# Kernel tuning notes

Hardware: AMD Instinct MI355X
Metric: run time of the kernel (lower is better)

The kernel has to match this reference:

```python
import jax, jax.numpy as jnp
import numpy as np

B, N, F, C = 8, 256, 59, 128
BOX = 20.0
EPS = 1e-5


def _bn(y, g, b, m, v):
    # eval-mode BatchNorm1d over the channel (last) axis
    return (y - m) * jax.lax.rsqrt(v + EPS) * g + b


def setup_inputs() -> dict:
    key = jax.random.key(0)
    ks = jax.random.split(key, 12)
    x = jax.random.normal(ks[0], (B, N, F), jnp.float32)
    pos = jax.random.uniform(ks[1], (B, N, 3), jnp.float32) * BOX
    nrm = jax.random.normal(ks[2], (B, N, 3), jnp.float32)
    normal = nrm / jnp.linalg.norm(nrm, axis=-1, keepdims=True)
    s_in = 1.0 / np.sqrt(F)
    W_lin = jax.random.normal(ks[3], (C, F), jnp.float32) * s_in
    W_src = jax.random.normal(ks[4], (C, F), jnp.float32) * s_in
    W_dst = jax.random.normal(ks[5], (C, F), jnp.float32) * s_in
    pos_w = jax.random.normal(ks[6], (C, 6), jnp.float32) * (1.0 / np.sqrt(6.0))
    pos_b = jax.random.normal(ks[7], (C,), jnp.float32) * 0.02
    attn_w = jax.random.normal(ks[8], (C, C), jnp.float32) * (1.0 / np.sqrt(C))
    attn_b = jax.random.normal(ks[9], (C,), jnp.float32) * 0.02
    pos_bn_g = 1.0 + 0.1 * jax.random.normal(ks[10], (C,), jnp.float32)
    attn_bn_g = 1.0 + 0.1 * jax.random.normal(ks[11], (C,), jnp.float32)
    zeros = jnp.zeros((C,), jnp.float32)
    ones = jnp.ones((C,), jnp.float32)
    return {
        'x': x, 'pos': pos, 'normal': normal,
        'W_lin': W_lin, 'W_src': W_src, 'W_dst': W_dst,
        'pos_w': pos_w, 'pos_b': pos_b,
        'pos_bn_g': pos_bn_g, 'pos_bn_b': zeros, 'pos_bn_m': zeros, 'pos_bn_v': ones,
        'attn_w': attn_w, 'attn_b': attn_b,
        'attn_bn_g': attn_bn_g, 'attn_bn_b': zeros, 'attn_bn_m': zeros, 'attn_bn_v': ones,
        'r': 5,
    }


def reference(x, pos, normal, W_lin, W_src, W_dst, pos_w, pos_b,
              pos_bn_g, pos_bn_b, pos_bn_m, pos_bn_v,
              attn_w, attn_b, attn_bn_g, attn_bn_b, attn_bn_m, attn_bn_v, r):
    r = jnp.float32(r)
    # linear projections (bias-free, as in PyG PointTransformerConv)
    v = jnp.einsum('bnf,cf->bnc', x, W_lin)      # values
    a_src = jnp.einsum('bnf,cf->bnc', x, W_src)  # alpha for source j
    a_dst = jnp.einsum('bnf,cf->bnc', x, W_dst)  # alpha for dest   i
    # relative geometry, axis 1 = receiver i, axis 2 = sender j
    rel_pos = pos[:, :, None, :] - pos[:, None, :, :]          # [B,i,j,3]
    rel_nrm = normal[:, :, None, :] - normal[:, None, :, :]    # [B,i,j,3]
    relf = jnp.concatenate([rel_pos, rel_nrm], axis=-1)        # [B,i,j,6]
    # pos_nn = Linear(6,C) + BN + ReLU (eval)
    delta = jax.nn.relu(_bn(jnp.einsum('bijk,ck->bijc', relf, pos_w) + pos_b,
                            pos_bn_g, pos_bn_b, pos_bn_m, pos_bn_v))
    # attn_nn(alpha_i - alpha_j + delta)
    alpha_arg = a_dst[:, :, None, :] - a_src[:, None, :, :] + delta
    scores = jax.nn.relu(_bn(jnp.einsum('bijc,dc->bijd', alpha_arg, attn_w) + attn_b,
                             attn_bn_g, attn_bn_b, attn_bn_m, attn_bn_v))
    # radius mask within each graph (self-loops included, dist 0 <= r)
    dist2 = jnp.sum(rel_pos * rel_pos, axis=-1)                # [B,i,j]
    mask = (dist2 <= r * r)[..., None]                         # [B,i,j,1]
    attn = jax.nn.softmax(jnp.where(mask, scores, -jnp.inf), axis=2)
    # per-channel vector attention over neighbors j: sum_j attn * (v_j + delta)
    out = jnp.sum(attn * (v[:, None, :, :] + delta), axis=2)   # [B,i,C]
    return out
```

## Files before the change

kernel.cpp:

```cpp
#include <hip/hip_runtime.h>

#define BB 8
#define NN 256
#define FF 59
#define CC 128
#define EPSV 1e-5f

#define WS_V     0
#define WS_ASRC  (WS_V + BB*NN*CC)
#define WS_ADST  (WS_ASRC + BB*NN*CC)
#define WS_PWT   (WS_ADST + BB*NN*CC)
#define WS_T1    (WS_PWT + 6*CC)
#define WS_T2    (WS_T1 + CC)
#define WS_WT    (WS_T2 + CC)

__global__ __launch_bounds__(256) void prep_kernel(
    const float* __restrict__ x, const float* __restrict__ W_lin,
    const float* __restrict__ W_src, const float* __restrict__ W_dst,
    const float* __restrict__ pos_w, const float* __restrict__ pos_b,
    const float* __restrict__ pos_g, const float* __restrict__ pos_bb,
    const float* __restrict__ pos_m, const float* __restrict__ pos_v,
    const float* __restrict__ attn_w, const float* __restrict__ attn_b,
    const float* __restrict__ attn_g, const float* __restrict__ attn_bb,
    const float* __restrict__ attn_m, const float* __restrict__ attn_v,
    float* __restrict__ ws)
{
    int blk = blockIdx.x;
    int tid = threadIdx.x;
    if (blk < 384) {
        int type = blk >> 7;
        int g    = blk & 127;
        int b    = g >> 4;
        int n0   = (g & 15) * 16;
        const float* W = (type == 0) ? W_lin : (type == 1) ? W_src : W_dst;
        float* outp = ws + ((type == 0) ? WS_V : (type == 1) ? WS_ASRC : WS_ADST);
        __shared__ float Wl[CC * FF];
        __shared__ float xs[16 * FF];
        for (int idx = tid; idx < CC * FF; idx += 256) Wl[idx] = W[idx];
        const float* xrow = x + (size_t)(b * NN + n0) * FF;
        for (int idx = tid; idx < 16 * FF; idx += 256) xs[idx] = xrow[idx];
        __syncthreads();
        int c = tid & 127, h = tid >> 7;
        float acc[8];
#pragma unroll
        for (int q = 0; q < 8; ++q) acc[q] = 0.f;
        for (int f = 0; f < FF; ++f) {
            float w = Wl[c * FF + f];
#pragma unroll
            for (int q = 0; q < 8; ++q) acc[q] += w * xs[(h * 8 + q) * FF + f];
        }
#pragma unroll
        for (int q = 0; q < 8; ++q) {
            int n = n0 + h * 8 + q;
            outp[(b * NN + n) * CC + c] = acc[q];
        }
    } else {
        __shared__ float S2s[CC];
        if (tid < CC) {
            int c = tid;
            float S1 = rsqrtf(pos_v[c] + EPSV) * pos_g[c];
            ws[WS_T1 + c] = (pos_b[c] - pos_m[c]) * S1 + pos_bb[c];
#pragma unroll
            for (int k = 0; k < 6; ++k) ws[WS_PWT + k * CC + c] = pos_w[c * 6 + k] * S1;
            float S2 = rsqrtf(attn_v[c] + EPSV) * attn_g[c];
            S2s[c] = S2;
            ws[WS_T2 + c] = (attn_b[c] - attn_m[c]) * S2 + attn_bb[c];
        }
        __syncthreads();
        for (int idx = tid; idx < CC * CC; idx += 256) {
            int d = idx & 127, cc2 = idx >> 7;
            ws[WS_WT + cc2 * CC + d] = attn_w[d * CC + cc2] * S2s[d];
        }
    }
}

__global__ __launch_bounds__(256) void main_kernel(
    const float* __restrict__ pos, const float* __restrict__ nrm,
    const int* __restrict__ rptr, const float* __restrict__ ws,
    float* __restrict__ out)
{
    const float* v    = ws + WS_V;
    const float* asrc = ws + WS_ASRC;
    const float* adst = ws + WS_ADST;
    const float* pwt  = ws + WS_PWT;
    const float* T1   = ws + WS_T1;
    const float* T2   = ws + WS_T2;
    const float* wt   = ws + WS_WT;

    int blk = blockIdx.x;
    int b = blk >> 8, i = blk & 255;
    int tid = threadIdx.x;

    __shared__ float relf[NN * 6];
    __shared__ int   jlist[NN];
    __shared__ int   wcnt[4];
    __shared__ int   cnt_s;
    __shared__ float alpha_t[CC * 20];
    __shared__ float u_lds[16 * CC];
    __shared__ float sered[CC], ored[CC];

    int rv = rptr[0];
    float r2 = (float)(rv * rv);
    const float* pib = pos + (size_t)(b * NN + i) * 3;
    const float* nib = nrm + (size_t)(b * NN + i) * 3;
    float pix = pib[0], piy = pib[1], piz = pib[2];
    float nix = nib[0], niy = nib[1], niz = nib[2];
    {
        int j = tid;
        const float* pj = pos + (size_t)(b * NN + j) * 3;
        const float* nj = nrm + (size_t)(b * NN + j) * 3;
        float dx = pix - pj[0], dy = piy - pj[1], dz = piz - pj[2];
        float ex = nix - nj[0], ey = niy - nj[1], ez = niz - nj[2];
        float d2 = dx * dx + dy * dy + dz * dz;
        bool valid = (d2 <= r2);
        unsigned long long m = __ballot(valid);
        int w = tid >> 6, lane = tid & 63;
        if (lane == 0) wcnt[w] = __popcll(m);
        __syncthreads();
        int off = 0;
        for (int w2 = 0; w2 < w; ++w2) off += wcnt[w2];
        if (tid == 0) cnt_s = wcnt[0] + wcnt[1] + wcnt[2] + wcnt[3];
        int rank = __popcll(m & ((1ull << lane) - 1ull));
        if (valid) {
            int s = off + rank;
            jlist[s] = j;
            relf[s * 6 + 0] = dx; relf[s * 6 + 1] = dy; relf[s * 6 + 2] = dz;
            relf[s * 6 + 3] = ex; relf[s * 6 + 4] = ey; relf[s * 6 + 5] = ez;
        }
    }
    __syncthreads();
    int cnt = cnt_s;

    int c    = tid & 127;
    int half = tid >> 7;

    float pw[6];
#pragma unroll
    for (int k = 0; k < 6; ++k) pw[k] = pwt[k * CC + c];
    float T1c    = T1[c];
    float T2d    = T2[c];
    float adst_c = adst[(b * NN + i) * CC + c];

    float se = 0.f, ov = 0.f;

    for (int base = 0; base < cnt; base += 16) {
        int tcnt = min(16, cnt - base);
#pragma unroll
        for (int q = 0; q < 8; ++q) {
            int js = half * 8 + q;
            float aval = 0.f, uval = 0.f;
            if (js < tcnt) {
                int j = jlist[base + js];
                const float* rf = &relf[(base + js) * 6];
                float dsum = T1c;
#pragma unroll
                for (int k = 0; k < 6; ++k) dsum += pw[k] * rf[k];
                float delta = fmaxf(dsum, 0.f);
                float as = asrc[(b * NN + j) * CC + c];
                float vv = v[(b * NN + j) * CC + c];
                aval = adst_c - as + delta;
                uval = vv + delta;
            }
            alpha_t[c * 20 + js] = aval;
            u_lds[js * CC + c]   = uval;
        }
        __syncthreads();
        if (half * 8 < tcnt) {
            float acc[8];
#pragma unroll
            for (int q = 0; q < 8; ++q) acc[q] = T2d;
            const float* wtp = wt + c;
#pragma unroll 4
            for (int cc2 = 0; cc2 < CC; ++cc2) {
                float wv = wtp[cc2 * CC];
                const float* ap = &alpha_t[cc2 * 20 + half * 8];
                float4 a0 = *(const float4*)ap;
                float4 a1 = *(const float4*)(ap + 4);
                acc[0] += a0.x * wv; acc[1] += a0.y * wv;
                acc[2] += a0.z * wv; acc[3] += a0.w * wv;
                acc[4] += a1.x * wv; acc[5] += a1.y * wv;
                acc[6] += a1.z * wv; acc[7] += a1.w * wv;
            }
#pragma unroll
            for (int q = 0; q < 8; ++q) {
                int js = half * 8 + q;
                if (js < tcnt) {
                    float s = fmaxf(acc[q], 0.f);
                    float e = __expf(s);
                    se += e;
                    ov += e * u_lds[js * CC + c];
                }
            }
        }
        __syncthreads();
    }

    if (half == 1) { sered[c] = se; ored[c] = ov; }
    __syncthreads();
    if (half == 0) {
        float S = se + sered[c];
        float O = ov + ored[c];
        out[(size_t)(b * NN + i) * CC + c] = O / S;
    }
}

extern "C" void kernel_launch(void* const* d_in, const int* in_sizes, int n_in,
                              void* d_out, int out_size, void* d_ws, size_t ws_size,
                              hipStream_t stream) {
    const float* x      = (const float*)d_in[0];
    const float* pos    = (const float*)d_in[1];
    const float* normal = (const float*)d_in[2];
    const float* W_lin  = (const float*)d_in[3];
    const float* W_src  = (const float*)d_in[4];
    const float* W_dst  = (const float*)d_in[5];
    const float* pos_w  = (const float*)d_in[6];
    const float* pos_b  = (const float*)d_in[7];
    const float* pos_g  = (const float*)d_in[8];
    const float* pos_bb = (const float*)d_in[9];
    const float* pos_m  = (const float*)d_in[10];
    const float* pos_v  = (const float*)d_in[11];
    const float* attn_w = (const float*)d_in[12];
    const float* attn_b = (const float*)d_in[13];
    const float* attn_g = (const float*)d_in[14];
    const float* attn_bb= (const float*)d_in[15];
    const float* attn_m = (const float*)d_in[16];
    const float* attn_v = (const float*)d_in[17];
    const int*   rptr   = (const int*)d_in[18];
    float* ws  = (float*)d_ws;
    float* out = (float*)d_out;

    prep_kernel<<<dim3(385), dim3(256), 0, stream>>>(
        x, W_lin, W_src, W_dst, pos_w, pos_b, pos_g, pos_bb, pos_m, pos_v,
        attn_w, attn_b, attn_g, attn_bb, attn_m, attn_v, ws);
    main_kernel<<<dim3(2048), dim3(256), 0, stream>>>(pos, normal, rptr, ws, out);
}
```

Measured before the change: 135.1 us.

## Use fp16 dot2 for attention matmul and keep u values in registers

Stores the BN-folded attention weight matrix as packed fp16 pairs and stages alpha in LDS as fp16, so the 128x128 attention product uses packed dot2 instructions that take two products per instruction. The u values now stay in registers instead of going through LDS. The prep projection pads F to 60 so it can use float4 loads. This trades fp32 accuracy in the attention scores for less LDS traffic and fewer multiply instructions. fp16 rounding ahead of exp may hurt tolerance.

```diff
diff --git a/kernel.cpp b/kernel.cpp
--- a/kernel.cpp
+++ b/kernel.cpp
@@ -1,4 +1,7 @@
 #include <hip/hip_runtime.h>
+
+typedef _Float16 h2 __attribute__((ext_vector_type(2)));
+typedef unsigned int uint32;
 
 #define BB 8
 #define NN 256
@@ -12,7 +15,20 @@
 #define WS_PWT   (WS_ADST + BB*NN*CC)
 #define WS_T1    (WS_PWT + 6*CC)
 #define WS_T2    (WS_T1 + CC)
-#define WS_WT    (WS_T2 + CC)
+#define WS_WTH   (WS_T2 + CC)
+
+#if __has_builtin(__builtin_amdgcn_fdot2)
+#define FDOT2(a, b, c) __builtin_amdgcn_fdot2((a), (b), (c), false)
+#else
+static __device__ __forceinline__ float fdot2_emul(h2 a, h2 b, float c) {
+    return c + (float)a.x * (float)b.x + (float)a.y * (float)b.y;
+}
+#define FDOT2 fdot2_emul
+#endif
+
+static __device__ __forceinline__ h2 as_h2(uint32 u) {
+    return __builtin_bit_cast(h2, u);
+}
 
 __global__ __launch_bounds__(256) void prep_kernel(
     const float* __restrict__ x, const float* __restrict__ W_lin,
@@ -34,20 +50,33 @@
         int n0   = (g & 15) * 16;
         const float* W = (type == 0) ? W_lin : (type == 1) ? W_src : W_dst;
         float* outp = ws + ((type == 0) ? WS_V : (type == 1) ? WS_ASRC : WS_ADST);
-        __shared__ float Wl[CC * FF];
-        __shared__ float xs[16 * FF];
-        for (int idx = tid; idx < CC * FF; idx += 256) Wl[idx] = W[idx];
+        __shared__ float Wl[CC * 60];
+        __shared__ float xs[16 * 60];
+        for (int idx = tid; idx < CC * 60; idx += 256) {
+            int r = idx / 60, f = idx - r * 60;
+            Wl[idx] = (f < FF) ? W[r * FF + f] : 0.f;
+        }
         const float* xrow = x + (size_t)(b * NN + n0) * FF;
-        for (int idx = tid; idx < 16 * FF; idx += 256) xs[idx] = xrow[idx];
+        for (int idx = tid; idx < 16 * 60; idx += 256) {
+            int r = idx / 60, f = idx - r * 60;
+            xs[idx] = (f < FF) ? xrow[r * FF + f] : 0.f;
+        }
         __syncthreads();
         int c = tid & 127, h = tid >> 7;
         float acc[8];
 #pragma unroll
         for (int q = 0; q < 8; ++q) acc[q] = 0.f;
-        for (int f = 0; f < FF; ++f) {
-            float w = Wl[c * FF + f];
-#pragma unroll
-            for (int q = 0; q < 8; ++q) acc[q] += w * xs[(h * 8 + q) * FF + f];
+#pragma unroll 3
+        for (int f4 = 0; f4 < 15; ++f4) {
+            float4 wq = *(const float4*)&Wl[c * 60 + f4 * 4];
+#pragma unroll
+            for (int q = 0; q < 8; ++q) {
+                float4 xq = *(const float4*)&xs[(h * 8 + q) * 60 + f4 * 4];
+                acc[q] = fmaf(wq.x, xq.x, acc[q]);
+                acc[q] = fmaf(wq.y, xq.y, acc[q]);
+                acc[q] = fmaf(wq.z, xq.z, acc[q]);
+                acc[q] = fmaf(wq.w, xq.w, acc[q]);
+            }
         }
 #pragma unroll
         for (int q = 0; q < 8; ++q) {
@@ -67,9 +96,15 @@
             ws[WS_T2 + c] = (attn_b[c] - attn_m[c]) * S2 + attn_bb[c];
         }
         __syncthreads();
-        for (int idx = tid; idx < CC * CC; idx += 256) {
-            int d = idx & 127, cc2 = idx >> 7;
-            ws[WS_WT + cc2 * CC + d] = attn_w[d * CC + cc2] * S2s[d];
+        uint32* wthp = (uint32*)ws + WS_WTH;
+        for (int idx = tid; idx < 64 * CC; idx += 256) {
+            int p = idx & 63, d = idx >> 6;
+            float s = S2s[d];
+            float2 w2 = *(const float2*)&attn_w[d * CC + 2 * p];
+            h2 hv;
+            hv.x = (_Float16)(w2.x * s);
+            hv.y = (_Float16)(w2.y * s);
+            wthp[p * CC + d] = __builtin_bit_cast(uint32, hv);
         }
     }
 }
@@ -85,7 +120,7 @@
     const float* pwt  = ws + WS_PWT;
     const float* T1   = ws + WS_T1;
     const float* T2   = ws + WS_T2;
-    const float* wt   = ws + WS_WT;
+    const uint32* wth = (const uint32*)ws + WS_WTH;
 
     int blk = blockIdx.x;
     int b = blk >> 8, i = blk & 255;
@@ -95,8 +130,7 @@
     __shared__ int   jlist[NN];
     __shared__ int   wcnt[4];
     __shared__ int   cnt_s;
-    __shared__ float alpha_t[CC * 20];
-    __shared__ float u_lds[16 * CC];
+    __shared__ _Float16 alpha_h[16 * 136];
     __shared__ float sered[CC], ored[CC];
 
     int rv = rptr[0];
@@ -145,50 +179,65 @@
 
     for (int base = 0; base < cnt; base += 16) {
         int tcnt = min(16, cnt - base);
-#pragma unroll
-        for (int q = 0; q < 8; ++q) {
-            int js = half * 8 + q;
-            float aval = 0.f, uval = 0.f;
-            if (js < tcnt) {
-                int j = jlist[base + js];
-                const float* rf = &relf[(base + js) * 6];
-                float dsum = T1c;
-#pragma unroll
-                for (int k = 0; k < 6; ++k) dsum += pw[k] * rf[k];
-                float delta = fmaxf(dsum, 0.f);
-                float as = asrc[(b * NN + j) * CC + c];
-                float vv = v[(b * NN + j) * CC + c];
-                aval = adst_c - as + delta;
-                uval = vv + delta;
-            }
-            alpha_t[c * 20 + js] = aval;
-            u_lds[js * CC + c]   = uval;
-        }
-        __syncthreads();
-        if (half * 8 < tcnt) {
+        int myn  = tcnt - half * 8;
+        float u_reg[8];
+        {
+            const int4* jp = (const int4*)&jlist[base + half * 8];
+            int4 ja = jp[0], jb4 = jp[1];
+            int jarr[8] = {ja.x, ja.y, ja.z, ja.w, jb4.x, jb4.y, jb4.z, jb4.w};
+            const float4* rp = (const float4*)&relf[(base + half * 8) * 6];
+            float rf[48];
+#pragma unroll
+            for (int t = 0; t < 12; ++t) {
+                float4 xx = rp[t];
+                rf[4 * t + 0] = xx.x; rf[4 * t + 1] = xx.y;
+                rf[4 * t + 2] = xx.z; rf[4 * t + 3] = xx.w;
+            }
+#pragma unroll
+            for (int q = 0; q < 8; ++q) {
+                float aval = 0.f, uval = 0.f;
+                if (q < myn) {
+                    int j = jarr[q];
+                    float dsum = T1c;
+#pragma unroll
+                    for (int k = 0; k < 6; ++k) dsum = fmaf(pw[k], rf[q * 6 + k], dsum);
+                    float delta = fmaxf(dsum, 0.f);
+                    aval = adst_c - asrc[(b * NN + j) * CC + c] + delta;
+                    uval = v[(b * NN + j) * CC + c] + delta;
+                }
+                alpha_h[(half * 8 + q) * 136 + c] = (_Float16)aval;
+                u_reg[q] = uval;
+            }
+        }
+        __syncthreads();
+        if (myn > 0) {
             float acc[8];
 #pragma unroll
             for (int q = 0; q < 8; ++q) acc[q] = T2d;
-            const float* wtp = wt + c;
+            const uint32* wp = wth + c;
 #pragma unroll 4
-            for (int cc2 = 0; cc2 < CC; ++cc2) {
-                float wv = wtp[cc2 * CC];
-                const float* ap = &alpha_t[cc2 * 20 + half * 8];
-                float4 a0 = *(const float4*)ap;
-                float4 a1 = *(const float4*)(ap + 4);
-                acc[0] += a0.x * wv; acc[1] += a0.y * wv;
-                acc[2] += a0.z * wv; acc[3] += a0.w * wv;
-                acc[4] += a1.x * wv; acc[5] += a1.y * wv;
-                acc[6] += a1.z * wv; acc[7] += a1.w * wv;
+            for (int co = 0; co < 16; ++co) {
+                uint32 w0 = wp[(co * 4 + 0) * CC];
+                uint32 w1 = wp[(co * 4 + 1) * CC];
+                uint32 w2 = wp[(co * 4 + 2) * CC];
+                uint32 w3 = wp[(co * 4 + 3) * CC];
+                h2 h0 = as_h2(w0), h1 = as_h2(w1), hh2 = as_h2(w2), h3 = as_h2(w3);
+#pragma unroll
+                for (int q = 0; q < 8; ++q) {
+                    uint4 av = *(const uint4*)&alpha_h[(half * 8 + q) * 136 + co * 8];
+                    acc[q] = FDOT2(as_h2(av.x), h0, acc[q]);
+                    acc[q] = FDOT2(as_h2(av.y), h1, acc[q]);
+                    acc[q] = FDOT2(as_h2(av.z), hh2, acc[q]);
+                    acc[q] = FDOT2(as_h2(av.w), h3, acc[q]);
+                }
             }
 #pragma unroll
             for (int q = 0; q < 8; ++q) {
-                int js = half * 8 + q;
-                if (js < tcnt) {
+                if (q < myn) {
                     float s = fmaxf(acc[q], 0.f);
                     float e = __expf(s);
                     se += e;
-                    ov += e * u_lds[js * CC + c];
+                    ov += e * u_reg[q];
                 }
             }
         }
```

Measured after the change: 131.4 us. 1.03x faster.
